# Kernel tuning notes

Hardware: AMD Instinct MI355X
Metric: run time of the kernel (lower is better)

Reference implementation:

```python
import jax, jax.numpy as jnp
import numpy as np

B, E, H, O = 131072, 32, 32, 2

def setup_inputs() -> dict:
    key = jax.random.key(0)
    ks = jax.random.split(key, 12)
    f32 = jnp.float32
    inp = {
        "last_pos_rel": jax.random.normal(ks[0], (B, O), dtype=f32),
        "hidden_state": jax.random.normal(ks[1], (1, B, H), dtype=f32),
        "start_pos": jax.random.normal(ks[2], (B, O), dtype=f32),
        # spatial embedding Linear(2 -> 32)
        "W_se": jax.random.normal(ks[3], (E, O), dtype=f32) * 0.1,
        "b_se": jax.random.normal(ks[4], (E,), dtype=f32) * 0.1,
        # LSTM (input E -> hidden H), PyTorch layout: [4H, E] / [4H, H], gate order i,f,g,o
        "W_ih": jax.random.normal(ks[5], (4 * H, E), dtype=f32) * 0.1,
        "b_ih": jax.random.normal(ks[6], (4 * H,), dtype=f32) * 0.1,
        "W_hh": jax.random.normal(ks[7], (4 * H, H), dtype=f32) * 0.1,
        "b_hh": jax.random.normal(ks[8], (4 * H,), dtype=f32) * 0.1,
        # hidden2pos Linear(32 -> 2)
        "W_hp": jax.random.normal(ks[9], (O, H), dtype=f32) * 0.1,
        "b_hp": jax.random.normal(ks[10], (O,), dtype=f32) * 0.1,
        "seq_len": 60,
    }
    return inp


def reference(last_pos_rel, hidden_state, start_pos, W_se, b_se,
              W_ih, b_ih, W_hh, b_hh, W_hp, b_hp, seq_len):
    # dropout in eval mode -> identity
    h0 = hidden_state[0]                     # (B, H)  num_layers == 1
    c0 = jnp.zeros_like(h0)
    x0 = last_pos_rel @ W_se.T + b_se        # (B, E) spatial embedding
    b_gate = b_ih + b_hh                     # (4H,)

    def step(carry, _):
        h, c, x = carry
        gates = x @ W_ih.T + h @ W_hh.T + b_gate          # (B, 4H)
        i, f, g, o = jnp.split(gates, 4, axis=-1)         # PyTorch gate order
        c = jax.nn.sigmoid(f) * c + jax.nn.sigmoid(i) * jnp.tanh(g)
        h = jax.nn.sigmoid(o) * jnp.tanh(c)
        pos_rel = h @ W_hp.T + b_hp                        # (B, 2)
        x_next = pos_rel @ W_se.T + b_se                   # feed prediction back
        return (h, c, x_next), pos_rel

    (hT, cT, _), pred_traj_rel = jax.lax.scan(step, (h0, c0, x0), None, length=seq_len)
    # relative_to_abs: cumsum over time, add start_pos
    abs_traj = jnp.cumsum(pred_traj_rel, axis=0) + start_pos[None, :, :]  # (T, B, 2)
    return abs_traj, hT[None, :, :]
```

## Files before the change

kernel.cpp:

```cpp
#include <hip/hip_runtime.h>

typedef _Float16 half8  __attribute__((ext_vector_type(8)));
typedef __fp16   half2v __attribute__((ext_vector_type(2)));
typedef float    f32x4  __attribute__((ext_vector_type(4)));
typedef float    f32x2  __attribute__((ext_vector_type(2)));

#define L2E 1.44269504088896340736f
#define MFMA(a, b, c) __builtin_amdgcn_mfma_f32_16x16x32_f16((a), (b), (c), 0, 0, 0)

__global__ void precompute_kernel(const float* __restrict__ W_se,
                                  const float* __restrict__ b_se,
                                  const float* __restrict__ W_ih,
                                  const float* __restrict__ b_ih,
                                  const float* __restrict__ W_hh,
                                  const float* __restrict__ b_hh,
                                  const float* __restrict__ W_hp,
                                  const float* __restrict__ b_hp,
                                  float* __restrict__ ws) {
    int s = threadIdx.x;
    if (s >= 128) return;
    if (s < 64) {
        int colp = s & 15, qp = s >> 4;
        unsigned int* dst = (unsigned int*)ws + 8704 + s * 4;
        for (int pp = 0; pp < 4; ++pp) {
            float v0 = (colp < 2) ? W_hp[colp * 32 + 8 * qp + 2 * pp]     : 0.f;
            float v1 = (colp < 2) ? W_hp[colp * 32 + 8 * qp + 2 * pp + 1] : 0.f;
            half2v h2 = __builtin_amdgcn_cvt_pkrtz(v0, v1);
            dst[pp] = __builtin_bit_cast(unsigned int, h2);
        }
    }
    int gi = s >> 5, hf = (s >> 4) & 1, q = (s >> 2) & 3, r = s & 3;
    int o  = gi * 32 + 8 * q + 4 * hf + r;
    float w0 = 0.f, w1 = 0.f, bse = 0.f;
    for (int e = 0; e < 32; ++e) {
        float wi = W_ih[o * 32 + e];
        w0  += W_se[e * 2 + 0] * wi;
        w1  += W_se[e * 2 + 1] * wi;
        bse += b_se[e] * wi;
    }
    float sc = (gi == 2) ? 2.0f * L2E : -L2E;
    for (int k = 0; k < 32; ++k) {
        float whh = W_hh[o * 32 + k];
        ws[s * 32 + k] = sc * (whh + W_hp[k] * w0 + W_hp[32 + k] * w1);
    }
    float bg = b_ih[o] + b_hh[o] + bse;
    ws[8192 + s] = sc * w0;
    ws[8320 + s] = sc * w1;
    ws[8448 + s] = sc * (bg + b_hp[0] * w0 + b_hp[1] * w1);
}

__device__ __forceinline__ void split8(const float* v, half8& hi, half8& lo) {
    #pragma unroll
    for (int p = 0; p < 4; ++p) {
        half2v hp = __builtin_amdgcn_cvt_pkrtz(v[2 * p], v[2 * p + 1]);
        hi[2 * p] = hp.x; hi[2 * p + 1] = hp.y;
        float l0 = v[2 * p]     - (float)hp.x;
        float l1 = v[2 * p + 1] - (float)hp.y;
        half2v lp2 = __builtin_amdgcn_cvt_pkrtz(l0, l1);
        lo[2 * p] = lp2.x; lo[2 * p + 1] = lp2.y;
    }
}

__global__ __launch_bounds__(256, 4) void lstm_kernel(
        const float* __restrict__ lp,
        const float* __restrict__ h0g,
        const float* __restrict__ sp,
        const float* __restrict__ bhp,
        const float* __restrict__ ws,
        const int*   __restrict__ seqp,
        float* __restrict__ out, int Bn) {
    __shared__ f32x4 wh_lds[8][64];

    const int tid  = threadIdx.x;
    const int lane = tid & 63;
    const int col  = lane & 15;
    const int q    = lane >> 4;
    int base = (blockIdx.x * 4 + (tid >> 6)) * 16;
    if (base + 16 > Bn) base = (Bn >= 16) ? (Bn - 16) : 0;
    const int T = seqp[0];

    const float* Wcs  = ws;
    const float* W00s = ws + 8192;
    const float* W01s = ws + 8320;
    const float* bg2q = ws + 8448 + 4 * q;
    const float* phb  = ws + 8704;

    if (tid < 64) {
        #pragma unroll
        for (int t8 = 0; t8 < 8; ++t8) {
            const float* p = Wcs + (size_t)(t8 * 16 + (tid & 15)) * 32 + 8 * (tid >> 4);
            half8 w;
            #pragma unroll
            for (int pp = 0; pp < 4; ++pp) {
                half2v h2 = __builtin_amdgcn_cvt_pkrtz(p[2 * pp], p[2 * pp + 1]);
                w[2 * pp] = h2.x; w[2 * pp + 1] = h2.y;
            }
            wh_lds[t8][tid] = __builtin_bit_cast(f32x4, w);
        }
    }
    __syncthreads();

    #define WHT(t8) __builtin_bit_cast(half8, *(volatile const f32x4*)&wh_lds[(t8)][lane])

    half8 pht = __builtin_bit_cast(half8, *(const f32x4*)(phb + lane * 4));
    const float pb0 = (q == 0) ? bhp[0] : 0.f;
    const float pb1 = (q == 0) ? bhp[1] : 0.f;

    f32x4 accg[8];
    {
        half8 b0h, b0l;
        {
            float v[8];
            const float* p = h0g + (size_t)(base + col) * 32 + 8 * q;
            #pragma unroll
            for (int i = 0; i < 8; ++i) v[i] = p[i];
            split8(v, b0h, b0l);
        }
        f32x4 ap;
        ap[0] = pb0; ap[1] = pb1; ap[2] = 0.f; ap[3] = 0.f;
        ap = MFMA(pht, b0h, ap);
        ap = MFMA(pht, b0l, ap);
        half8 dh;
        #pragma unroll
        for (int i = 0; i < 8; ++i) dh[i] = (_Float16)0.f;
        if (q == 0) {
            float d0 = lp[(size_t)(base + col) * 2 + 0] - ap[0];
            float d1 = lp[(size_t)(base + col) * 2 + 1] - ap[1];
            half2v x = __builtin_amdgcn_cvt_pkrtz(d0, d1);
            dh[0] = x.x; dh[1] = x.y;
        }
        #pragma unroll
        for (int t8 = 0; t8 < 8; ++t8) {
            f32x4 a = *(const f32x4*)(bg2q + t8 * 16);
            a = MFMA(WHT(t8), b0h, a);
            a = MFMA(WHT(t8), b0l, a);
            half8 ch;
            #pragma unroll
            for (int i = 0; i < 8; ++i) ch[i] = (_Float16)0.f;
            if (q == 0) {
                half2v y = __builtin_amdgcn_cvt_pkrtz(W00s[t8 * 16 + col],
                                                      W01s[t8 * 16 + col]);
                ch[0] = y.x; ch[1] = y.y;
            }
            a = MFMA(ch, dh, a);
            accg[t8] = a;
        }
    }

    f32x2 c2[4];
    #pragma unroll
    for (int i = 0; i < 4; ++i) c2[i] = (f32x2)0.f;
    float run0 = 0.f, run1 = 0.f;
    if (q == 0) {
        run0 = sp[(size_t)(base + col) * 2 + 0];
        run1 = sp[(size_t)(base + col) * 2 + 1];
    }

    half8 bh;

    #pragma unroll 1
    for (int n = 0; n < T; ++n) {
        #pragma unroll
        for (int hf = 0; hf < 2; ++hf) {
            #pragma unroll
            for (int rp = 0; rp < 2; ++rp) {
                const int idx = 2 * hf + rp;
                f32x2 gI, gF, gG, gO;
                gI.x = accg[0 + hf][2 * rp]; gI.y = accg[0 + hf][2 * rp + 1];
                gF.x = accg[2 + hf][2 * rp]; gF.y = accg[2 + hf][2 * rp + 1];
                gG.x = accg[4 + hf][2 * rp]; gG.y = accg[4 + hf][2 * rp + 1];
                gO.x = accg[6 + hf][2 * rp]; gO.y = accg[6 + hf][2 * rp + 1];
                f32x2 ei, ef, eg, eo;
                ei.x = __builtin_amdgcn_exp2f(gI.x); ei.y = __builtin_amdgcn_exp2f(gI.y);
                ef.x = __builtin_amdgcn_exp2f(gF.x); ef.y = __builtin_amdgcn_exp2f(gF.y);
                eg.x = __builtin_amdgcn_exp2f(gG.x); eg.y = __builtin_amdgcn_exp2f(gG.y);
                eo.x = __builtin_amdgcn_exp2f(gO.x); eo.y = __builtin_amdgcn_exp2f(gO.y);
                f32x2 Df = ef + 1.f;
                f32x2 P  = (ei + 1.f) * (eg + 1.f);
                f32x2 PD = P * Df;
                f32x2 R;
                R.x = __builtin_amdgcn_rcpf(PD.x); R.y = __builtin_amdgcn_rcpf(PD.y);
                f32x2 cn = ((eg - 1.f) * Df + c2[idx] * P) * R;
                c2[idx] = cn;
                f32x2 arg = cn * (2.f * L2E);
                f32x2 ec;
                ec.x = __builtin_amdgcn_exp2f(arg.x); ec.y = __builtin_amdgcn_exp2f(arg.y);
                f32x2 DDo = (ec + 1.f) * (eo + 1.f);
                f32x2 Rs;
                Rs.x = __builtin_amdgcn_rcpf(DDo.x); Rs.y = __builtin_amdgcn_rcpf(DDo.y);
                f32x2 h2 = (ec - 1.f) * Rs;
                half2v hp = __builtin_amdgcn_cvt_pkrtz(h2.x, h2.y);
                bh[2 * idx] = hp.x; bh[2 * idx + 1] = hp.y;
            }
        }

        f32x4 ap;
        ap[0] = pb0; ap[1] = pb1; ap[2] = 0.f; ap[3] = 0.f;
        ap = MFMA(pht, bh, ap);

        #pragma unroll
        for (int t8 = 0; t8 < 8; ++t8) {
            f32x4 a = *(const f32x4*)(bg2q + t8 * 16);
            accg[t8] = MFMA(WHT(t8), bh, a);
        }

        if (q == 0) {
            run0 += ap[0]; run1 += ap[1];
            float2 w2; w2.x = run0; w2.y = run1;
            *(float2*)(out + 2 * ((size_t)n * Bn + base + col)) = w2;
        }
    }

    {
        float* p = out + (size_t)T * Bn * 2 + (size_t)(base + col) * 32 + 8 * q;
        float4 v0, v1;
        v0.x = (float)bh[0]; v0.y = (float)bh[1]; v0.z = (float)bh[2]; v0.w = (float)bh[3];
        v1.x = (float)bh[4]; v1.y = (float)bh[5]; v1.z = (float)bh[6]; v1.w = (float)bh[7];
        *(float4*)(p)     = v0;
        *(float4*)(p + 4) = v1;
    }
    #undef WHT
}

extern "C" void kernel_launch(void* const* d_in, const int* in_sizes, int n_in,
                              void* d_out, int out_size, void* d_ws, size_t ws_size,
                              hipStream_t stream) {
    const float* last_pos_rel = (const float*)d_in[0];
    const float* hidden_state = (const float*)d_in[1];
    const float* start_pos    = (const float*)d_in[2];
    const float* W_se         = (const float*)d_in[3];
    const float* b_se         = (const float*)d_in[4];
    const float* W_ih         = (const float*)d_in[5];
    const float* b_ih         = (const float*)d_in[6];
    const float* W_hh         = (const float*)d_in[7];
    const float* b_hh         = (const float*)d_in[8];
    const float* W_hp         = (const float*)d_in[9];
    const float* b_hp         = (const float*)d_in[10];
    const int*   seq_len      = (const int*)d_in[11];

    float* out = (float*)d_out;
    float* ws  = (float*)d_ws;

    const int Bn = in_sizes[0] / 2;

    hipLaunchKernelGGL(precompute_kernel, dim3(1), dim3(128), 0, stream,
                       W_se, b_se, W_ih, b_ih, W_hh, b_hh, W_hp, b_hp, ws);

    const int ntiles = (Bn + 15) / 16;
    const int nblk   = (ntiles + 3) / 4;
    hipLaunchKernelGGL(lstm_kernel, dim3(nblk), dim3(256), 0, stream,
                       last_pos_rel, hidden_state, start_pos, b_hp,
                       ws, seq_len, out, Bn);
}
```

Baseline: 198.6 us.

## Process two independent 16-row batch tiles per wave to interleave recurrences

Each wave now carries two independent LSTM batch tiles through the time loop. Their activations and MFMAs are interleaved, and each weight fragment read from LDS is reused for both tiles. The goal is to hide the serial MFMA→activation dependency latency with independent work and to halve LDS weight reads per tile. The cost is roughly double the register state, so launch bounds are lowered from 4 to 3 blocks per SM, which reduces occupancy and halves the grid size.

```diff
diff --git a/kernel.cpp b/kernel.cpp
--- a/kernel.cpp
+++ b/kernel.cpp
@@ -61,7 +61,7 @@
     }
 }
 
-__global__ __launch_bounds__(256, 4) void lstm_kernel(
+__global__ __launch_bounds__(256, 3) void lstm_kernel(
         const float* __restrict__ lp,
         const float* __restrict__ h0g,
         const float* __restrict__ sp,
@@ -75,8 +75,9 @@
     const int lane = tid & 63;
     const int col  = lane & 15;
     const int q    = lane >> 4;
-    int base = (blockIdx.x * 4 + (tid >> 6)) * 16;
-    if (base + 16 > Bn) base = (Bn >= 16) ? (Bn - 16) : 0;
+    int baseA = (blockIdx.x * 4 + (tid >> 6)) * 32;
+    if (baseA + 32 > Bn) baseA = (Bn >= 32) ? (Bn - 32) : 0;
+    const int baseB = baseA + 16;
     const int T = seqp[0];
 
     const float* Wcs  = ws;
@@ -106,8 +107,11 @@
     const float pb0 = (q == 0) ? bhp[0] : 0.f;
     const float pb1 = (q == 0) ? bhp[1] : 0.f;
 
-    f32x4 accg[8];
-    {
+    f32x4 accgA[8], accgB[8];
+    #pragma unroll
+    for (int tile = 0; tile < 2; ++tile) {
+        const int  base = tile ? baseB : baseA;
+        f32x4*     accg = tile ? accgB : accgA;
         half8 b0h, b0l;
         {
             float v[8];
@@ -132,8 +136,9 @@
         #pragma unroll
         for (int t8 = 0; t8 < 8; ++t8) {
             f32x4 a = *(const f32x4*)(bg2q + t8 * 16);
-            a = MFMA(WHT(t8), b0h, a);
-            a = MFMA(WHT(t8), b0l, a);
+            half8 w = WHT(t8);
+            a = MFMA(w, b0h, a);
+            a = MFMA(w, b0l, a);
             half8 ch;
             #pragma unroll
             for (int i = 0; i < 8; ++i) ch[i] = (_Float16)0.f;
@@ -147,16 +152,48 @@
         }
     }
 
-    f32x2 c2[4];
+    f32x2 c2A[4], c2B[4];
     #pragma unroll
-    for (int i = 0; i < 4; ++i) c2[i] = (f32x2)0.f;
-    float run0 = 0.f, run1 = 0.f;
+    for (int i = 0; i < 4; ++i) { c2A[i] = (f32x2)0.f; c2B[i] = (f32x2)0.f; }
+    float runA0 = 0.f, runA1 = 0.f, runB0 = 0.f, runB1 = 0.f;
     if (q == 0) {
-        run0 = sp[(size_t)(base + col) * 2 + 0];
-        run1 = sp[(size_t)(base + col) * 2 + 1];
-    }
-
-    half8 bh;
+        runA0 = sp[(size_t)(baseA + col) * 2 + 0];
+        runA1 = sp[(size_t)(baseA + col) * 2 + 1];
+        runB0 = sp[(size_t)(baseB + col) * 2 + 0];
+        runB1 = sp[(size_t)(baseB + col) * 2 + 1];
+    }
+
+    half8 bhA, bhB;
+
+    auto act2 = [&](f32x4* accg, f32x2* c2, half8& bh, int hf, int rp) {
+        const int idx = 2 * hf + rp;
+        f32x2 gI, gF, gG, gO;
+        gI.x = accg[0 + hf][2 * rp]; gI.y = accg[0 + hf][2 * rp + 1];
+        gF.x = accg[2 + hf][2 * rp]; gF.y = accg[2 + hf][2 * rp + 1];
+        gG.x = accg[4 + hf][2 * rp]; gG.y = accg[4 + hf][2 * rp + 1];
+        gO.x = accg[6 + hf][2 * rp]; gO.y = accg[6 + hf][2 * rp + 1];
+        f32x2 ei, ef, eg, eo;
+        ei.x = __builtin_amdgcn_exp2f(gI.x); ei.y = __builtin_amdgcn_exp2f(gI.y);
+        ef.x = __builtin_amdgcn_exp2f(gF.x); ef.y = __builtin_amdgcn_exp2f(gF.y);
+        eg.x = __builtin_amdgcn_exp2f(gG.x); eg.y = __builtin_amdgcn_exp2f(gG.y);
+        eo.x = __builtin_amdgcn_exp2f(gO.x); eo.y = __builtin_amdgcn_exp2f(gO.y);
+        f32x2 Df = ef + 1.f;
+        f32x2 P  = (ei + 1.f) * (eg + 1.f);
+        f32x2 PD = P * Df;
+        f32x2 R;
+        R.x = __builtin_amdgcn_rcpf(PD.x); R.y = __builtin_amdgcn_rcpf(PD.y);
+        f32x2 cn = ((eg - 1.f) * Df + c2[idx] * P) * R;
+        c2[idx] = cn;
+        f32x2 arg = cn * (2.f * L2E);
+        f32x2 ec;
+        ec.x = __builtin_amdgcn_exp2f(arg.x); ec.y = __builtin_amdgcn_exp2f(arg.y);
+        f32x2 DDo = (ec + 1.f) * (eo + 1.f);
+        f32x2 Rs;
+        Rs.x = __builtin_amdgcn_rcpf(DDo.x); Rs.y = __builtin_amdgcn_rcpf(DDo.y);
+        f32x2 h2 = (ec - 1.f) * Rs;
+        half2v hp = __builtin_amdgcn_cvt_pkrtz(h2.x, h2.y);
+        bh[2 * idx] = hp.x; bh[2 * idx + 1] = hp.y;
+    };
 
     #pragma unroll 1
     for (int n = 0; n < T; ++n) {
@@ -164,60 +201,47 @@
         for (int hf = 0; hf < 2; ++hf) {
             #pragma unroll
             for (int rp = 0; rp < 2; ++rp) {
-                const int idx = 2 * hf + rp;
-                f32x2 gI, gF, gG, gO;
-                gI.x = accg[0 + hf][2 * rp]; gI.y = accg[0 + hf][2 * rp + 1];
-                gF.x = accg[2 + hf][2 * rp]; gF.y = accg[2 + hf][2 * rp + 1];
-                gG.x = accg[4 + hf][2 * rp]; gG.y = accg[4 + hf][2 * rp + 1];
-                gO.x = accg[6 + hf][2 * rp]; gO.y = accg[6 + hf][2 * rp + 1];
-                f32x2 ei, ef, eg, eo;
-                ei.x = __builtin_amdgcn_exp2f(gI.x); ei.y = __builtin_amdgcn_exp2f(gI.y);
-                ef.x = __builtin_amdgcn_exp2f(gF.x); ef.y = __builtin_amdgcn_exp2f(gF.y);
-                eg.x = __builtin_amdgcn_exp2f(gG.x); eg.y = __builtin_amdgcn_exp2f(gG.y);
-                eo.x = __builtin_amdgcn_exp2f(gO.x); eo.y = __builtin_amdgcn_exp2f(gO.y);
-                f32x2 Df = ef + 1.f;
-                f32x2 P  = (ei + 1.f) * (eg + 1.f);
-                f32x2 PD = P * Df;
-                f32x2 R;
-                R.x = __builtin_amdgcn_rcpf(PD.x); R.y = __builtin_amdgcn_rcpf(PD.y);
-                f32x2 cn = ((eg - 1.f) * Df + c2[idx] * P) * R;
-                c2[idx] = cn;
-                f32x2 arg = cn * (2.f * L2E);
-                f32x2 ec;
-                ec.x = __builtin_amdgcn_exp2f(arg.x); ec.y = __builtin_amdgcn_exp2f(arg.y);
-                f32x2 DDo = (ec + 1.f) * (eo + 1.f);
-                f32x2 Rs;
-                Rs.x = __builtin_amdgcn_rcpf(DDo.x); Rs.y = __builtin_amdgcn_rcpf(DDo.y);
-                f32x2 h2 = (ec - 1.f) * Rs;
-                half2v hp = __builtin_amdgcn_cvt_pkrtz(h2.x, h2.y);
-                bh[2 * idx] = hp.x; bh[2 * idx + 1] = hp.y;
+                act2(accgA, c2A, bhA, hf, rp);
+                act2(accgB, c2B, bhB, hf, rp);
             }
         }
 
-        f32x4 ap;
-        ap[0] = pb0; ap[1] = pb1; ap[2] = 0.f; ap[3] = 0.f;
-        ap = MFMA(pht, bh, ap);
+        f32x4 apA, apB;
+        apA[0] = pb0; apA[1] = pb1; apA[2] = 0.f; apA[3] = 0.f;
+        apB = apA;
+        apA = MFMA(pht, bhA, apA);
+        apB = MFMA(pht, bhB, apB);
 
         #pragma unroll
         for (int t8 = 0; t8 < 8; ++t8) {
-            f32x4 a = *(const f32x4*)(bg2q + t8 * 16);
-            accg[t8] = MFMA(WHT(t8), bh, a);
+            f32x4 bt = *(const f32x4*)(bg2q + t8 * 16);
+            half8 w  = WHT(t8);
+            accgA[t8] = MFMA(w, bhA, bt);
+            accgB[t8] = MFMA(w, bhB, bt);
         }
 
         if (q == 0) {
-            run0 += ap[0]; run1 += ap[1];
-            float2 w2; w2.x = run0; w2.y = run1;
-            *(float2*)(out + 2 * ((size_t)n * Bn + base + col)) = w2;
+            runA0 += apA[0]; runA1 += apA[1];
+            runB0 += apB[0]; runB1 += apB[1];
+            float2 wA; wA.x = runA0; wA.y = runA1;
+            float2 wB; wB.x = runB0; wB.y = runB1;
+            *(float2*)(out + 2 * ((size_t)n * Bn + baseA + col)) = wA;
+            *(float2*)(out + 2 * ((size_t)n * Bn + baseB + col)) = wB;
         }
     }
 
     {
-        float* p = out + (size_t)T * Bn * 2 + (size_t)(base + col) * 32 + 8 * q;
+        float* pa = out + (size_t)T * Bn * 2 + (size_t)(baseA + col) * 32 + 8 * q;
+        float* pb = out + (size_t)T * Bn * 2 + (size_t)(baseB + col) * 32 + 8 * q;
         float4 v0, v1;
-        v0.x = (float)bh[0]; v0.y = (float)bh[1]; v0.z = (float)bh[2]; v0.w = (float)bh[3];
-        v1.x = (float)bh[4]; v1.y = (float)bh[5]; v1.z = (float)bh[6]; v1.w = (float)bh[7];
-        *(float4*)(p)     = v0;
-        *(float4*)(p + 4) = v1;
+        v0.x = (float)bhA[0]; v0.y = (float)bhA[1]; v0.z = (float)bhA[2]; v0.w = (float)bhA[3];
+        v1.x = (float)bhA[4]; v1.y = (float)bhA[5]; v1.z = (float)bhA[6]; v1.w = (float)bhA[7];
+        *(float4*)(pa)     = v0;
+        *(float4*)(pa + 4) = v1;
+        v0.x = (float)bhB[0]; v0.y = (float)bhB[1]; v0.z = (float)bhB[2]; v0.w = (float)bhB[3];
+        v1.x = (float)bhB[4]; v1.y = (float)bhB[5]; v1.z = (float)bhB[6]; v1.w = (float)bhB[7];
+        *(float4*)(pb)     = v0;
+        *(float4*)(pb + 4) = v1;
     }
     #undef WHT
 }
@@ -246,8 +270,8 @@
     hipLaunchKernelGGL(precompute_kernel, dim3(1), dim3(128), 0, stream,
                        W_se, b_se, W_ih, b_ih, W_hh, b_hh, W_hp, b_hp, ws);
 
-    const int ntiles = (Bn + 15) / 16;
-    const int nblk   = (ntiles + 3) / 4;
+    const int npairs = (Bn + 31) / 32;
+    const int nblk   = (npairs + 3) / 4;
     hipLaunchKernelGGL(lstm_kernel, dim3(nblk), dim3(256), 0, stream,
                        last_pos_rel, hidden_state, start_pos, b_hp,
                        ws, seq_len, out, Bn);
```

Result: slower. 223.0 us (+12.3%).

## Split recurrent MFMA into K=16 halves to overlap with gate activations

Applied to the files above, without the earlier changes.

Splits the per-step recurrent 16x16x32 MFMA into two 16x16x16 MFMAs over the lower and upper halves of the hidden vector. Matrix work on the first half starts while the activations for the second half are still being computed, so the matrix unit and the vector ALU can overlap within a step. Gate biases are moved from global memory into LDS. The cost is twice as many MFMA issues, each with lower throughput per instruction, plus more register pressure from the held upper weight halves.

```diff
diff --git a/kernel.cpp b/kernel.cpp
--- a/kernel.cpp
+++ b/kernel.cpp
@@ -1,12 +1,14 @@
 #include <hip/hip_runtime.h>
 
 typedef _Float16 half8  __attribute__((ext_vector_type(8)));
+typedef _Float16 half4  __attribute__((ext_vector_type(4)));
 typedef __fp16   half2v __attribute__((ext_vector_type(2)));
 typedef float    f32x4  __attribute__((ext_vector_type(4)));
 typedef float    f32x2  __attribute__((ext_vector_type(2)));
 
 #define L2E 1.44269504088896340736f
-#define MFMA(a, b, c) __builtin_amdgcn_mfma_f32_16x16x32_f16((a), (b), (c), 0, 0, 0)
+#define MFMA(a, b, c)   __builtin_amdgcn_mfma_f32_16x16x32_f16((a), (b), (c), 0, 0, 0)
+#define MFMA16(a, b, c) __builtin_amdgcn_mfma_f32_16x16x16f16((a), (b), (c), 0, 0, 0)
 
 __global__ void precompute_kernel(const float* __restrict__ W_se,
                                   const float* __restrict__ b_se,
@@ -70,6 +72,7 @@
         const int*   __restrict__ seqp,
         float* __restrict__ out, int Bn) {
     __shared__ f32x4 wh_lds[8][64];
+    __shared__ f32x4 bias_lds[32];
 
     const int tid  = threadIdx.x;
     const int lane = tid & 63;
@@ -82,7 +85,6 @@
     const float* Wcs  = ws;
     const float* W00s = ws + 8192;
     const float* W01s = ws + 8320;
-    const float* bg2q = ws + 8448 + 4 * q;
     const float* phb  = ws + 8704;
 
     if (tid < 64) {
@@ -97,12 +99,18 @@
             }
             wh_lds[t8][tid] = __builtin_bit_cast(f32x4, w);
         }
+    } else if (tid >= 128 && tid < 160) {
+        bias_lds[tid - 128] = *(const f32x4*)(ws + 8448 + (tid - 128) * 4);
     }
     __syncthreads();
 
     #define WHT(t8) __builtin_bit_cast(half8, *(volatile const f32x4*)&wh_lds[(t8)][lane])
+    #define BIA(t8) (*(volatile const f32x4*)&bias_lds[(t8) * 4 + q])
+    #define LO4(w)  __builtin_shufflevector((w), (w), 0, 1, 2, 3)
+    #define HI4(w)  __builtin_shufflevector((w), (w), 4, 5, 6, 7)
 
     half8 pht = __builtin_bit_cast(half8, *(const f32x4*)(phb + lane * 4));
+    const half4 phlo = LO4(pht), phhi = HI4(pht);
     const float pb0 = (q == 0) ? bhp[0] : 0.f;
     const float pb1 = (q == 0) ? bhp[1] : 0.f;
 
@@ -131,9 +139,10 @@
         }
         #pragma unroll
         for (int t8 = 0; t8 < 8; ++t8) {
-            f32x4 a = *(const f32x4*)(bg2q + t8 * 16);
-            a = MFMA(WHT(t8), b0h, a);
-            a = MFMA(WHT(t8), b0l, a);
+            f32x4 a = BIA(t8);
+            half8 w = WHT(t8);
+            a = MFMA(w, b0h, a);
+            a = MFMA(w, b0l, a);
             half8 ch;
             #pragma unroll
             for (int i = 0; i < 8; ++i) ch[i] = (_Float16)0.f;
@@ -156,53 +165,70 @@
         run1 = sp[(size_t)(base + col) * 2 + 1];
     }
 
-    half8 bh;
+    half4 bhlo, bhhi;
+
+    auto act2 = [&](f32x4* accg_, half4& bhh, int hf, int rp) {
+        const int idx = 2 * hf + rp;
+        f32x2 gI, gF, gG, gO;
+        gI.x = accg_[0 + hf][2 * rp]; gI.y = accg_[0 + hf][2 * rp + 1];
+        gF.x = accg_[2 + hf][2 * rp]; gF.y = accg_[2 + hf][2 * rp + 1];
+        gG.x = accg_[4 + hf][2 * rp]; gG.y = accg_[4 + hf][2 * rp + 1];
+        gO.x = accg_[6 + hf][2 * rp]; gO.y = accg_[6 + hf][2 * rp + 1];
+        f32x2 ei, ef, eg, eo;
+        ei.x = __builtin_amdgcn_exp2f(gI.x); ei.y = __builtin_amdgcn_exp2f(gI.y);
+        ef.x = __builtin_amdgcn_exp2f(gF.x); ef.y = __builtin_amdgcn_exp2f(gF.y);
+        eg.x = __builtin_amdgcn_exp2f(gG.x); eg.y = __builtin_amdgcn_exp2f(gG.y);
+        eo.x = __builtin_amdgcn_exp2f(gO.x); eo.y = __builtin_amdgcn_exp2f(gO.y);
+        f32x2 Df = ef + 1.f;
+        f32x2 P  = (ei + 1.f) * (eg + 1.f);
+        f32x2 PD = P * Df;
+        f32x2 R;
+        R.x = __builtin_amdgcn_rcpf(PD.x); R.y = __builtin_amdgcn_rcpf(PD.y);
+        f32x2 cn = ((eg - 1.f) * Df + c2[idx] * P) * R;
+        c2[idx] = cn;
+        f32x2 arg = cn * (2.f * L2E);
+        f32x2 ec;
+        ec.x = __builtin_amdgcn_exp2f(arg.x); ec.y = __builtin_amdgcn_exp2f(arg.y);
+        f32x2 DDo = (ec + 1.f) * (eo + 1.f);
+        f32x2 Rs;
+        Rs.x = __builtin_amdgcn_rcpf(DDo.x); Rs.y = __builtin_amdgcn_rcpf(DDo.y);
+        f32x2 h2 = (ec - 1.f) * Rs;
+        half2v hp = __builtin_amdgcn_cvt_pkrtz(h2.x, h2.y);
+        bhh[2 * rp] = hp.x; bhh[2 * rp + 1] = hp.y;
+    };
 
     #pragma unroll 1
     for (int n = 0; n < T; ++n) {
-        #pragma unroll
-        for (int hf = 0; hf < 2; ++hf) {
-            #pragma unroll
-            for (int rp = 0; rp < 2; ++rp) {
-                const int idx = 2 * hf + rp;
-                f32x2 gI, gF, gG, gO;
-                gI.x = accg[0 + hf][2 * rp]; gI.y = accg[0 + hf][2 * rp + 1];
-                gF.x = accg[2 + hf][2 * rp]; gF.y = accg[2 + hf][2 * rp + 1];
-                gG.x = accg[4 + hf][2 * rp]; gG.y = accg[4 + hf][2 * rp + 1];
-                gO.x = accg[6 + hf][2 * rp]; gO.y = accg[6 + hf][2 * rp + 1];
-                f32x2 ei, ef, eg, eo;
-                ei.x = __builtin_amdgcn_exp2f(gI.x); ei.y = __builtin_amdgcn_exp2f(gI.y);
-                ef.x = __builtin_amdgcn_exp2f(gF.x); ef.y = __builtin_amdgcn_exp2f(gF.y);
-                eg.x = __builtin_amdgcn_exp2f(gG.x); eg.y = __builtin_amdgcn_exp2f(gG.y);
-                eo.x = __builtin_amdgcn_exp2f(gO.x); eo.y = __builtin_amdgcn_exp2f(gO.y);
-                f32x2 Df = ef + 1.f;
-                f32x2 P  = (ei + 1.f) * (eg + 1.f);
-                f32x2 PD = P * Df;
-                f32x2 R;
-                R.x = __builtin_amdgcn_rcpf(PD.x); R.y = __builtin_amdgcn_rcpf(PD.y);
-                f32x2 cn = ((eg - 1.f) * Df + c2[idx] * P) * R;
-                c2[idx] = cn;
-                f32x2 arg = cn * (2.f * L2E);
-                f32x2 ec;
-                ec.x = __builtin_amdgcn_exp2f(arg.x); ec.y = __builtin_amdgcn_exp2f(arg.y);
-                f32x2 DDo = (ec + 1.f) * (eo + 1.f);
-                f32x2 Rs;
-                Rs.x = __builtin_amdgcn_rcpf(DDo.x); Rs.y = __builtin_amdgcn_rcpf(DDo.y);
-                f32x2 h2 = (ec - 1.f) * Rs;
-                half2v hp = __builtin_amdgcn_cvt_pkrtz(h2.x, h2.y);
-                bh[2 * idx] = hp.x; bh[2 * idx + 1] = hp.y;
-            }
-        }
+        act2(accg, bhlo, 0, 0);
+        act2(accg, bhlo, 0, 1);
+
+        half4 whiE[4];
+        #pragma unroll
+        for (int e = 0; e < 4; ++e) {
+            const int t8 = 2 * e;
+            half8 w = WHT(t8);
+            whiE[e] = HI4(w);
+            accg[t8] = MFMA16(LO4(w), bhlo, BIA(t8));
+        }
+
+        act2(accg, bhhi, 1, 0);
+        act2(accg, bhhi, 1, 1);
 
         f32x4 ap;
         ap[0] = pb0; ap[1] = pb1; ap[2] = 0.f; ap[3] = 0.f;
-        ap = MFMA(pht, bh, ap);
-
-        #pragma unroll
-        for (int t8 = 0; t8 < 8; ++t8) {
-            f32x4 a = *(const f32x4*)(bg2q + t8 * 16);
-            accg[t8] = MFMA(WHT(t8), bh, a);
-        }
+        ap = MFMA16(phlo, bhlo, ap);
+        ap = MFMA16(phhi, bhhi, ap);
+
+        #pragma unroll
+        for (int e = 0; e < 4; ++e) {
+            const int t8 = 2 * e + 1;
+            half8 w = WHT(t8);
+            f32x4 a = MFMA16(LO4(w), bhlo, BIA(t8));
+            accg[t8] = MFMA16(HI4(w), bhhi, a);
+        }
+        #pragma unroll
+        for (int e = 0; e < 4; ++e)
+            accg[2 * e] = MFMA16(whiE[e], bhhi, accg[2 * e]);
 
         if (q == 0) {
             run0 += ap[0]; run1 += ap[1];
@@ -214,12 +240,15 @@
     {
         float* p = out + (size_t)T * Bn * 2 + (size_t)(base + col) * 32 + 8 * q;
         float4 v0, v1;
-        v0.x = (float)bh[0]; v0.y = (float)bh[1]; v0.z = (float)bh[2]; v0.w = (float)bh[3];
-        v1.x = (float)bh[4]; v1.y = (float)bh[5]; v1.z = (float)bh[6]; v1.w = (float)bh[7];
+        v0.x = (float)bhlo[0]; v0.y = (float)bhlo[1]; v0.z = (float)bhlo[2]; v0.w = (float)bhlo[3];
+        v1.x = (float)bhhi[0]; v1.y = (float)bhhi[1]; v1.z = (float)bhhi[2]; v1.w = (float)bhhi[3];
         *(float4*)(p)     = v0;
         *(float4*)(p + 4) = v1;
     }
     #undef WHT
+    #undef BIA
+    #undef LO4
+    #undef HI4
 }
 
 extern "C" void kernel_launch(void* const* d_in, const int* in_sizes, int n_in,
```

Result: slower. 241.2 us (+21.4%).
